# Optimization experiments

Measured on AMD Instinct MI355X. Metric: run time of the kernel, lower is better.

## Reference

```python
import jax, jax.numpy as jnp
import numpy as np

B, T, F = 512, 256, 24
CF = 64            # cnn_filters
IN = 2 * CF        # LNN input size after second conv
UNITS = 128        # lnn_units
DENSE = 64         # dense_units
ODE_UNFOLDS = 6    # semi-implicit ODE solver unfolds (LiquidNet default)


def _maxpool1d(x):  # [B,C,T] -> [B,C,T//2]
    return jax.lax.reduce_window(x, -jnp.inf, jax.lax.max, (1, 1, 2), (1, 1, 2), 'VALID')


def setup_inputs() -> dict:
    key = jax.random.key(0)
    ks = jax.random.split(key, 16)
    u = lambda k, shape, lo, hi: jax.random.uniform(k, shape, jnp.float32, lo, hi)
    return {
        'x': jax.random.normal(ks[0], (B, T, F), jnp.float32),
        'conv1_w': jax.random.normal(ks[1], (CF, F, 5), jnp.float32) * 0.1,
        'conv1_b': jnp.zeros((CF,), jnp.float32),
        'conv2_w': jax.random.normal(ks[2], (2 * CF, CF, 3), jnp.float32) * 0.1,
        'conv2_b': jnp.zeros((2 * CF,), jnp.float32),
        'input_w': jnp.ones((IN,), jnp.float32),
        'input_b': jnp.zeros((IN,), jnp.float32),
        'sensory_mu': u(ks[3], (IN, UNITS), 0.3, 0.8),
        'sensory_sigma': u(ks[4], (IN, UNITS), 3.0, 8.0),
        'sensory_W': u(ks[5], (IN, UNITS), 0.01, 1.0),
        'sensory_erev': jnp.sign(jax.random.normal(ks[6], (IN, UNITS))).astype(jnp.float32),
        'mu': u(ks[7], (UNITS, UNITS), 0.3, 0.8),
        'sigma': u(ks[8], (UNITS, UNITS), 3.0, 8.0),
        'W': u(ks[9], (UNITS, UNITS), 0.01, 1.0),
        'erev': jnp.sign(jax.random.normal(ks[10], (UNITS, UNITS))).astype(jnp.float32),
        'vleak': u(ks[11], (UNITS,), -0.2, 0.2),
        'gleak': jnp.ones((UNITS,), jnp.float32),
        'cm_t': jnp.full((UNITS,), 0.5, jnp.float32),
        'fc1_w': jax.random.normal(ks[12], (DENSE, UNITS), jnp.float32) * 0.05,
        'fc1_b': jnp.zeros((DENSE,), jnp.float32),
        'fc2_w': jax.random.normal(ks[13], (1, DENSE), jnp.float32) * 0.05,
        'fc2_b': jnp.zeros((1,), jnp.float32),
    }


def _forward(x, conv1_w, conv1_b, conv2_w, conv2_b, input_w, input_b,
             sensory_mu, sensory_sigma, sensory_W, sensory_erev,
             mu, sigma, W, erev, vleak, gleak, cm_t,
             fc1_w, fc1_b, fc2_w, fc2_b):
    # --- CNN feature extractor ---
    h = jnp.transpose(x, (0, 2, 1))                        # [B, F, T]
    dn = ('NCH', 'OIH', 'NCH')
    h = jax.lax.conv_general_dilated(h, conv1_w, (1,), 'SAME', dimension_numbers=dn)
    h = _maxpool1d(jax.nn.relu(h + conv1_b[None, :, None]))
    h = jax.lax.conv_general_dilated(h, conv2_w, (1,), 'SAME', dimension_numbers=dn)
    h = _maxpool1d(jax.nn.relu(h + conv2_b[None, :, None]))  # dropout: eval mode (identity)
    feats = jnp.transpose(h, (0, 2, 1))                    # [B, T/4, IN]
    xs = jnp.transpose(feats, (1, 0, 2))                   # [T', B, IN] for scan

    # --- LiquidNet (LTC) recurrence, semi-implicit ODE solver ---
    def step(v, xt):
        xt = xt * input_w + input_b                        # affine input mapping
        s_act = sensory_W * jax.nn.sigmoid((xt[:, :, None] - sensory_mu) * sensory_sigma)  # [B,IN,U]
        w_num_s = jnp.sum(s_act * sensory_erev, axis=1)    # [B,U]
        w_den_s = jnp.sum(s_act, axis=1)
        for _ in range(ODE_UNFOLDS):
            w_act = W * jax.nn.sigmoid((v[:, :, None] - mu) * sigma)  # [B,U,U]
            w_num = jnp.sum(w_act * erev, axis=1) + w_num_s
            w_den = jnp.sum(w_act, axis=1) + w_den_s
            v = (cm_t * v + gleak * vleak + w_num) / (cm_t + gleak + w_den)
        return v, None

    h0 = jnp.zeros((x.shape[0], UNITS), x.dtype)
    hT, _ = jax.lax.scan(jax.checkpoint(step), h0, xs)

    # --- MLP head ---
    y = jax.nn.relu(hT @ fc1_w.T + fc1_b)
    return y @ fc2_w.T + fc2_b                             # [B, 1]


def reference(x, conv1_w, conv1_b, conv2_w, conv2_b, input_w, input_b,
              sensory_mu, sensory_sigma, sensory_W, sensory_erev,
              mu, sigma, W, erev, vleak, gleak, cm_t,
              fc1_w, fc1_b, fc2_w, fc2_b):
    return _forward(x, conv1_w, conv1_b, conv2_w, conv2_b, input_w, input_b,
                    sensory_mu, sensory_sigma, sensory_W, sensory_erev,
                    mu, sigma, W, erev, vleak, gleak, cm_t,
                    fc1_w, fc1_b, fc2_w, fc2_b)
```

## Files before the change

### kernel.cpp

```cpp
#include <hip/hip_runtime.h>
#include <hip/hip_bf16.h>


#define L2E 1.4426950408889634f

__global__ __launch_bounds__(256)
void prep_kernel(const float* __restrict__ smu, const float* __restrict__ ssig,
                 const float* __restrict__ sW,  const float* __restrict__ serev,
                 const float* __restrict__ mu,  const float* __restrict__ sig,
                 const float* __restrict__ W,   const float* __restrict__ erev,
                 const float* __restrict__ in_w, const float* __restrict__ in_b,
                 float2* __restrict__ R12T, float* __restrict__ VTT,
                 float2* __restrict__ S2T, float* __restrict__ SWT) {
  int idx = blockIdx.x * 256 + threadIdx.x;
  int i = idx >> 7, j = idx & 127;
  int h = i >> 4, n = i & 15;
  int dst = n * 1024 + j * 8 + h;
  float r1 = sig[idx] * L2E;
  R12T[dst] = make_float2(r1, mu[idx] * r1);
  VTT[dst]  = W[idx] * erev[idx];
  float ss = ssig[idx] * L2E;
  S2T[dst] = make_float2(ss * in_w[i], (smu[idx] - in_b[i]) * ss);
  SWT[dst] = sW[idx] * serev[idx];
}

__launch_bounds__(512)
__global__ void conv1_kernel(const float* __restrict__ x, const float* __restrict__ w1,
                             const float* __restrict__ b1, float* __restrict__ P1) {
  __shared__ float xs[6240];
  int tid = threadIdx.x, b = blockIdx.x;
  const float* xb = x + (size_t)b * 6144;
  for (int idx = tid; idx < 6144; idx += 512) xs[idx + 48] = xb[idx];
  if (tid < 48) { xs[tid] = 0.f; xs[6192 + tid] = 0.f; }
  __syncthreads();
  int tp = tid & 127, cq = tid >> 7;
  float acc0[16], acc1[16];
#pragma unroll
  for (int n = 0; n < 16; n++) { float bb = b1[cq * 16 + n]; acc0[n] = bb; acc1[n] = bb; }
  for (int cic = 0; cic < 3; cic++) {
    float p[6][8];
#pragma unroll
    for (int r = 0; r < 6; r++) {
      const float* row = &xs[(2 * tp + r) * 24 + cic * 8];
      float4 a = *(const float4*)row;
      float4 c = *(const float4*)(row + 4);
      p[r][0] = a.x; p[r][1] = a.y; p[r][2] = a.z; p[r][3] = a.w;
      p[r][4] = c.x; p[r][5] = c.y; p[r][6] = c.z; p[r][7] = c.w;
    }
#pragma unroll
    for (int n = 0; n < 16; n++) {
      const float* wr = w1 + (cq * 16 + n) * 120 + cic * 40;
#pragma unroll
      for (int c = 0; c < 8; c++) {
#pragma unroll
        for (int kk = 0; kk < 5; kk++) {
          float w = wr[c * 5 + kk];
          acc0[n] = fmaf(p[kk][c],     w, acc0[n]);
          acc1[n] = fmaf(p[kk + 1][c], w, acc1[n]);
        }
      }
    }
  }
  float* pb = P1 + (size_t)b * 8192;
#pragma unroll
  for (int n = 0; n < 16; n++)
    pb[(cq * 16 + n) * 128 + tp] = fmaxf(fmaxf(acc0[n], acc1[n]), 0.f);
}

__launch_bounds__(512)
__global__ void conv2_kernel(const float* __restrict__ P1, const float* __restrict__ w2,
                             const float* __restrict__ b2, float* __restrict__ feats) {
  __shared__ float xs[8450];
  int tid = threadIdx.x, b = blockIdx.x;
  const float* pb = P1 + (size_t)b * 8192;
  for (int idx = tid; idx < 8192; idx += 512) {
    int ci = idx >> 7, t = idx & 127;
    xs[(t + 1) * 65 + ci] = pb[idx];
  }
  if (tid < 65) { xs[tid] = 0.f; xs[129 * 65 + tid] = 0.f; }
  __syncthreads();
  int tp = tid & 63, cq = tid >> 6;
  float acc0[16], acc1[16];
#pragma unroll
  for (int n = 0; n < 16; n++) { float bb = b2[cq * 16 + n]; acc0[n] = bb; acc1[n] = bb; }
  for (int cic = 0; cic < 8; cic++) {
    float p[4][8];
#pragma unroll
    for (int r = 0; r < 4; r++)
#pragma unroll
      for (int c = 0; c < 8; c++)
        p[r][c] = xs[(2 * tp + r) * 65 + cic * 8 + c];
#pragma unroll
    for (int n = 0; n < 16; n++) {
      const float* wr = w2 + (cq * 16 + n) * 192 + cic * 24;
#pragma unroll
      for (int c = 0; c < 8; c++) {
#pragma unroll
        for (int kk = 0; kk < 3; kk++) {
          float w = wr[c * 3 + kk];
          acc0[n] = fmaf(p[kk][c],     w, acc0[n]);
          acc1[n] = fmaf(p[kk + 1][c], w, acc1[n]);
        }
      }
    }
  }
  __syncthreads();
#pragma unroll
  for (int n = 0; n < 16; n += 4) {
    float4 v;
    v.x = fmaxf(fmaxf(acc0[n],     acc1[n]),     0.f);
    v.y = fmaxf(fmaxf(acc0[n + 1], acc1[n + 1]), 0.f);
    v.z = fmaxf(fmaxf(acc0[n + 2], acc1[n + 2]), 0.f);
    v.w = fmaxf(fmaxf(acc0[n + 3], acc1[n + 3]), 0.f);
    *(float4*)&xs[tp * 128 + cq * 16 + n] = v;
  }
  __syncthreads();
  float* fb = feats + (size_t)b * 8192;
  for (int idx = tid; idx < 8192; idx += 512) fb[idx] = xs[idx];
}

__global__ void __launch_bounds__(1024) __attribute__((amdgpu_waves_per_eu(4, 4)))
lnn_kernel(const float2* __restrict__ R12T, const float* __restrict__ VTT,
           const float2* __restrict__ S2T, const float* __restrict__ SWT,
           const float* __restrict__ feats,
           const float* __restrict__ cm_t, const float* __restrict__ gleak,
           const float* __restrict__ vleak,
           const float* __restrict__ fc1_w, const float* __restrict__ fc1_b,
           const float* __restrict__ fc2_w, const float* __restrict__ fc2_b,
           float* __restrict__ out) {
  __shared__ float2 xt2[2][136];
  __shared__ float2 vbuf[2][136];
  __shared__ float red[2][64];
  int tid = threadIdx.x;
  int h = tid & 7, j = tid >> 3;
  int b0 = blockIdx.x * 2;

  float2 r12[16]; float vw[16], sw[16];
#pragma unroll
  for (int n = 0; n < 16; n++) {
    r12[n] = R12T[n * 1024 + tid];
    vw[n]  = VTT[n * 1024 + tid];
    sw[n]  = SWT[n * 1024 + tid];
  }

  float cmj = cm_t[j], glk = gleak[j];
  float gvl = glk * vleak[j], cgl = cmj + glk;
  float vj0 = 0.f, vj1 = 0.f;
  if (tid < 136) vbuf[0][tid] = make_float2(0.f, 0.f);
  const float* f0 = feats + (size_t)b0 * 8192;
  const float* f1 = f0 + 8192;
  if (tid < 128) xt2[0][tid + (tid >> 4)] = make_float2(f0[tid], f1[tid]);
  __syncthreads();

  const int hb = 17 * h;
  const float2* s2p = S2T + tid;

  for (int t = 0; t < 64; t++) {
    float pf0 = 0.f, pf1 = 0.f;
    if (tid < 128 && t < 63) {
      pf0 = f0[(t + 1) * 128 + tid];
      pf1 = f1[(t + 1) * 128 + tid];
    }

    float sn0 = 0.f, sd0 = 0.f, sn1 = 0.f, sd1 = 0.f;
    {
      const float2* xb = xt2[t & 1];
#pragma unroll 8
      for (int n = 0; n < 16; n++) {
        float2 s = s2p[n * 1024];
        float2 xv = xb[hb + n];
        float q0 = __builtin_amdgcn_rcpf(1.f + __builtin_amdgcn_exp2f(fmaf(-s.x, xv.x, s.y)));
        sn0 = fmaf(sw[n], q0, sn0); sd0 = fmaf(fabsf(sw[n]), q0, sd0);
        float q1 = __builtin_amdgcn_rcpf(1.f + __builtin_amdgcn_exp2f(fmaf(-s.x, xv.y, s.y)));
        sn1 = fmaf(sw[n], q1, sn1); sd1 = fmaf(fabsf(sw[n]), q1, sd1);
      }
    }

    for (int u = 0; u < 6; u++) {
      float n0 = sn0, d0 = sd0, n1 = sn1, d1 = sd1;
      const float2* vb = vbuf[u & 1] + hb;
#pragma unroll
      for (int n = 0; n < 16; n++) {
        float2 rr = r12[n];
        float2 v2 = vb[n];
        float q0 = __builtin_amdgcn_rcpf(1.f + __builtin_amdgcn_exp2f(fmaf(-rr.x, v2.x, rr.y)));
        n0 = fmaf(vw[n], q0, n0); d0 = fmaf(fabsf(vw[n]), q0, d0);
        float q1 = __builtin_amdgcn_rcpf(1.f + __builtin_amdgcn_exp2f(fmaf(-rr.x, v2.y, rr.y)));
        n1 = fmaf(vw[n], q1, n1); d1 = fmaf(fabsf(vw[n]), q1, d1);
      }
#pragma unroll
      for (int m = 1; m < 8; m <<= 1) {
        n0 += __shfl_xor(n0, m, 64);
        d0 += __shfl_xor(d0, m, 64);
        n1 += __shfl_xor(n1, m, 64);
        d1 += __shfl_xor(d1, m, 64);
      }
      if (u == 4 && tid < 128 && t < 63)
        xt2[(t + 1) & 1][tid + (tid >> 4)] = make_float2(pf0, pf1);
      if (h < 2) {
        float nn = h ? n1 : n0, dd = h ? d1 : d0;
        float vj = h ? vj1 : vj0;
        float den = cgl + dd;
        float ii = __builtin_amdgcn_rcpf(den); ii = ii * fmaf(-den, ii, 2.f);
        vj = (fmaf(cmj, vj, gvl) + nn) * ii;
        if (h) vj1 = vj; else vj0 = vj;
        ((float*)vbuf[(u + 1) & 1])[(j + (j >> 4)) * 2 + h] = vj;
      }
      __syncthreads();
    }
  }

  if (tid < 128) {
    int g = tid >> 6, d = tid & 63;
    float acc = fc1_b[d];
    for (int u = 0; u < 128; u++) {
      float2 v2 = vbuf[0][u + (u >> 4)];
      acc = fmaf(g ? v2.y : v2.x, fc1_w[d * 128 + u], acc);
    }
    red[g][d] = fmaxf(acc, 0.f) * fc2_w[d];
  }
  __syncthreads();
  if (tid < 2) {
    float s = fc2_b[0];
    for (int d = 0; d < 64; d++) s += red[tid][d];
    out[b0 + tid] = s;
  }
}

extern "C" void kernel_launch(void* const* d_in, const int* in_sizes, int n_in,
                              void* d_out, int out_size, void* d_ws, size_t ws_size,
                              hipStream_t stream) {
  (void)in_sizes; (void)n_in; (void)out_size; (void)ws_size;
  char* ws = (char*)d_ws;
  float*  P1   = (float*)(ws);
  float*  feats= (float*)(ws + (16 << 20));
  float2* R12T = (float2*)(ws + 0);
  float*  VTT  = (float*)(ws + (128 << 10));
  float2* S2T  = (float2*)(ws + (192 << 10));
  float*  SWT  = (float*)(ws + (320 << 10));

  conv1_kernel<<<512, 512, 0, stream>>>((const float*)d_in[0],
      (const float*)d_in[1], (const float*)d_in[2], P1);
  conv2_kernel<<<512, 512, 0, stream>>>(P1,
      (const float*)d_in[3], (const float*)d_in[4], feats);
  prep_kernel<<<64, 256, 0, stream>>>(
      (const float*)d_in[7], (const float*)d_in[8],
      (const float*)d_in[9], (const float*)d_in[10],
      (const float*)d_in[11], (const float*)d_in[12],
      (const float*)d_in[13], (const float*)d_in[14],
      (const float*)d_in[5], (const float*)d_in[6],
      R12T, VTT, S2T, SWT);
  lnn_kernel<<<256, 1024, 0, stream>>>(R12T, VTT, S2T, SWT, feats,
      (const float*)d_in[17], (const float*)d_in[16], (const float*)d_in[15],
      (const float*)d_in[18], (const float*)d_in[19],
      (const float*)d_in[20], (const float*)d_in[21],
      (float*)d_out);
}
```

Baseline: 1.277 ms.

## Process one sample per LNN block and reload weights from cache

The LNN recurrence kernel now handles one batch sample per 1024-thread block instead of two, doubling the grid. Synapse parameters are no longer held in registers; they are re-read from global memory (L1/L2) on every unfold, and all 64 timesteps of features are staged into shared memory up front instead of being prefetched per step. The waves-per-EU hint is raised to 8 so two blocks can share a CU, trading register-resident weights and two-sample amortization for higher occupancy and more memory traffic.

```diff
diff --git a/kernel.cpp b/kernel.cpp
--- a/kernel.cpp
+++ b/kernel.cpp
@@ -119,7 +119,7 @@
   for (int idx = tid; idx < 8192; idx += 512) fb[idx] = xs[idx];
 }
 
-__global__ void __launch_bounds__(1024) __attribute__((amdgpu_waves_per_eu(4, 4)))
+__global__ void __launch_bounds__(1024) __attribute__((amdgpu_waves_per_eu(8)))
 lnn_kernel(const float2* __restrict__ R12T, const float* __restrict__ VTT,
            const float2* __restrict__ S2T, const float* __restrict__ SWT,
            const float* __restrict__ feats,
@@ -128,102 +128,84 @@
            const float* __restrict__ fc1_w, const float* __restrict__ fc1_b,
            const float* __restrict__ fc2_w, const float* __restrict__ fc2_b,
            float* __restrict__ out) {
-  __shared__ float2 xt2[2][136];
-  __shared__ float2 vbuf[2][136];
-  __shared__ float red[2][64];
+  __shared__ float xt_all[64][136];
+  __shared__ float vbuf[2][136];
+  __shared__ float red[64];
   int tid = threadIdx.x;
   int h = tid & 7, j = tid >> 3;
-  int b0 = blockIdx.x * 2;
-
-  float2 r12[16]; float vw[16], sw[16];
-#pragma unroll
-  for (int n = 0; n < 16; n++) {
-    r12[n] = R12T[n * 1024 + tid];
-    vw[n]  = VTT[n * 1024 + tid];
-    sw[n]  = SWT[n * 1024 + tid];
+  int b = blockIdx.x;
+
+  {
+    const float* fb = feats + (size_t)b * 8192;
+    for (int idx = tid; idx < 8192; idx += 1024) {
+      int t = idx >> 7, u = idx & 127;
+      xt_all[t][u + (u >> 4)] = fb[idx];
+    }
   }
 
   float cmj = cm_t[j], glk = gleak[j];
   float gvl = glk * vleak[j], cgl = cmj + glk;
-  float vj0 = 0.f, vj1 = 0.f;
-  if (tid < 136) vbuf[0][tid] = make_float2(0.f, 0.f);
-  const float* f0 = feats + (size_t)b0 * 8192;
-  const float* f1 = f0 + 8192;
-  if (tid < 128) xt2[0][tid + (tid >> 4)] = make_float2(f0[tid], f1[tid]);
+  float vj = 0.f;
+  if (tid < 136) vbuf[0][tid] = 0.f;
   __syncthreads();
 
   const int hb = 17 * h;
   const float2* s2p = S2T + tid;
+  const float*  swp = SWT + tid;
+  const float2* rp  = R12T + tid;
+  const float*  vwp = VTT + tid;
 
   for (int t = 0; t < 64; t++) {
-    float pf0 = 0.f, pf1 = 0.f;
-    if (tid < 128 && t < 63) {
-      pf0 = f0[(t + 1) * 128 + tid];
-      pf1 = f1[(t + 1) * 128 + tid];
-    }
-
-    float sn0 = 0.f, sd0 = 0.f, sn1 = 0.f, sd1 = 0.f;
+    float sn = 0.f, sd = 0.f;
     {
-      const float2* xb = xt2[t & 1];
+      const float* xb = xt_all[t];
 #pragma unroll 8
       for (int n = 0; n < 16; n++) {
         float2 s = s2p[n * 1024];
-        float2 xv = xb[hb + n];
-        float q0 = __builtin_amdgcn_rcpf(1.f + __builtin_amdgcn_exp2f(fmaf(-s.x, xv.x, s.y)));
-        sn0 = fmaf(sw[n], q0, sn0); sd0 = fmaf(fabsf(sw[n]), q0, sd0);
-        float q1 = __builtin_amdgcn_rcpf(1.f + __builtin_amdgcn_exp2f(fmaf(-s.x, xv.y, s.y)));
-        sn1 = fmaf(sw[n], q1, sn1); sd1 = fmaf(fabsf(sw[n]), q1, sd1);
+        float w = swp[n * 1024];
+        float xv = xb[hb + n];
+        float q = __builtin_amdgcn_rcpf(1.f + __builtin_amdgcn_exp2f(fmaf(-s.x, xv, s.y)));
+        sn = fmaf(w, q, sn); sd = fmaf(fabsf(w), q, sd);
       }
     }
 
     for (int u = 0; u < 6; u++) {
-      float n0 = sn0, d0 = sd0, n1 = sn1, d1 = sd1;
-      const float2* vb = vbuf[u & 1] + hb;
+      float n0 = sn, d0 = sd;
+      const float* vb = vbuf[u & 1] + hb;
 #pragma unroll
       for (int n = 0; n < 16; n++) {
-        float2 rr = r12[n];
-        float2 v2 = vb[n];
-        float q0 = __builtin_amdgcn_rcpf(1.f + __builtin_amdgcn_exp2f(fmaf(-rr.x, v2.x, rr.y)));
-        n0 = fmaf(vw[n], q0, n0); d0 = fmaf(fabsf(vw[n]), q0, d0);
-        float q1 = __builtin_amdgcn_rcpf(1.f + __builtin_amdgcn_exp2f(fmaf(-rr.x, v2.y, rr.y)));
-        n1 = fmaf(vw[n], q1, n1); d1 = fmaf(fabsf(vw[n]), q1, d1);
+        float2 rr = rp[n * 1024];
+        float vw = vwp[n * 1024];
+        float v2 = vb[n];
+        float q = __builtin_amdgcn_rcpf(1.f + __builtin_amdgcn_exp2f(fmaf(-rr.x, v2, rr.y)));
+        n0 = fmaf(vw, q, n0); d0 = fmaf(fabsf(vw), q, d0);
       }
 #pragma unroll
       for (int m = 1; m < 8; m <<= 1) {
         n0 += __shfl_xor(n0, m, 64);
         d0 += __shfl_xor(d0, m, 64);
-        n1 += __shfl_xor(n1, m, 64);
-        d1 += __shfl_xor(d1, m, 64);
-      }
-      if (u == 4 && tid < 128 && t < 63)
-        xt2[(t + 1) & 1][tid + (tid >> 4)] = make_float2(pf0, pf1);
-      if (h < 2) {
-        float nn = h ? n1 : n0, dd = h ? d1 : d0;
-        float vj = h ? vj1 : vj0;
-        float den = cgl + dd;
+      }
+      if (h == 0) {
+        float den = cgl + d0;
         float ii = __builtin_amdgcn_rcpf(den); ii = ii * fmaf(-den, ii, 2.f);
-        vj = (fmaf(cmj, vj, gvl) + nn) * ii;
-        if (h) vj1 = vj; else vj0 = vj;
-        ((float*)vbuf[(u + 1) & 1])[(j + (j >> 4)) * 2 + h] = vj;
+        vj = (fmaf(cmj, vj, gvl) + n0) * ii;
+        vbuf[(u + 1) & 1][j + (j >> 4)] = vj;
       }
       __syncthreads();
     }
   }
 
-  if (tid < 128) {
-    int g = tid >> 6, d = tid & 63;
-    float acc = fc1_b[d];
-    for (int u = 0; u < 128; u++) {
-      float2 v2 = vbuf[0][u + (u >> 4)];
-      acc = fmaf(g ? v2.y : v2.x, fc1_w[d * 128 + u], acc);
-    }
-    red[g][d] = fmaxf(acc, 0.f) * fc2_w[d];
-  }
-  __syncthreads();
-  if (tid < 2) {
+  if (tid < 64) {
+    float acc = fc1_b[tid];
+    for (int u = 0; u < 128; u++)
+      acc = fmaf(vbuf[0][u + (u >> 4)], fc1_w[tid * 128 + u], acc);
+    red[tid] = fmaxf(acc, 0.f) * fc2_w[tid];
+  }
+  __syncthreads();
+  if (tid == 0) {
     float s = fc2_b[0];
-    for (int d = 0; d < 64; d++) s += red[tid][d];
-    out[b0 + tid] = s;
+    for (int d = 0; d < 64; d++) s += red[d];
+    out[b] = s;
   }
 }
 
@@ -250,7 +232,7 @@
       (const float*)d_in[13], (const float*)d_in[14],
       (const float*)d_in[5], (const float*)d_in[6],
       R12T, VTT, S2T, SWT);
-  lnn_kernel<<<256, 1024, 0, stream>>>(R12T, VTT, S2T, SWT, feats,
+  lnn_kernel<<<512, 1024, 0, stream>>>(R12T, VTT, S2T, SWT, feats,
       (const float*)d_in[17], (const float*)d_in[16], (const float*)d_in[15],
       (const float*)d_in[18], (const float*)d_in[19],
       (const float*)d_in[20], (const float*)d_in[21],
```

Result: slower. 1.591 ms (+24.6%).
